# Optimization experiments

Measured on AMD Instinct MI355X. Metric: run time of the kernel, lower is better.

The kernel has to match this reference:

```python
import jax, jax.numpy as jnp
import numpy as np

B, T, I, H, L, O = 2048, 512, 1, 64, 2, 1


def _lstm_layer(x, Wih, Whh, b):
    """Single LSTM layer, batch_first x: [B, T, in] -> [B, T, H].
    PyTorch gate order: i, f, g, o. b = b_ih + b_hh (folded)."""
    Bn = x.shape[0]
    Hn = Whh.shape[1]
    # Precompute input contribution for all timesteps (hoisted out of scan)
    xg = jnp.einsum('bti,gi->btg', x, Wih) + b  # [B, T, 4H]

    def step(carry, xg_t):
        h, c = carry
        g = xg_t + h @ Whh.T  # [B, 4H]
        i, f, gg, o = jnp.split(g, 4, axis=-1)
        i = jax.nn.sigmoid(i)
        f = jax.nn.sigmoid(f)
        gg = jnp.tanh(gg)
        o = jax.nn.sigmoid(o)
        c = f * c + i * gg
        h = o * jnp.tanh(c)
        return (h, c), h

    h0 = jnp.zeros((Bn, Hn), x.dtype)
    c0 = jnp.zeros((Bn, Hn), x.dtype)
    (_, _), hs = jax.lax.scan(step, (h0, c0), jnp.swapaxes(xg, 0, 1))  # hs: [T, B, H]
    return jnp.swapaxes(hs, 0, 1)


def setup_inputs() -> dict:
    key = jax.random.key(0)
    ks = jax.random.split(key, 11)
    s = 1.0 / np.sqrt(H)  # torch default uniform bound
    u = lambda k, shp: jax.random.uniform(k, shp, jnp.float32, -s, s)
    return {
        'x': jax.random.normal(ks[0], (B, T, I), jnp.float32),
        'Wih0': u(ks[1], (4 * H, I)),
        'Whh0': u(ks[2], (4 * H, H)),
        'bih0': u(ks[3], (4 * H,)),
        'bhh0': u(ks[4], (4 * H,)),
        'Wih1': u(ks[5], (4 * H, H)),
        'Whh1': u(ks[6], (4 * H, H)),
        'bih1': u(ks[7], (4 * H,)),
        'bhh1': u(ks[8], (4 * H,)),
        'fcW': u(ks[9], (O, H)),
        'fcb': u(ks[10], (O,)),
    }


def reference(x, Wih0, Whh0, bih0, bhh0, Wih1, Whh1, bih1, bhh1, fcW, fcb):
    h1 = _lstm_layer(x, Wih0, Whh0, bih0 + bhh0)   # [B, T, H]
    h2 = _lstm_layer(h1, Wih1, Whh1, bih1 + bhh1)  # [B, T, H]
    return h2[:, -1, :] @ fcW.T + fcb               # [B, O]
```

## Files before the change

kernel.cpp:

```cpp
#include <hip/hip_runtime.h>


#define TT 512
#define HH 64
#define BT 8

typedef __attribute__((ext_vector_type(4))) int i32x4;

#define MFMAI8 __builtin_amdgcn_mfma_i32_16x16x64_i8

#define WSCALE 260096.0f
#define HSCALE 32512.0f
#define LOG2E  1.44269504f
constexpr float C_SIG = (float)(256.0 / (260096.0 * 32512.0) * 1.4426950408889634);
constexpr float C_TGH = (float)(2.0 * 256.0 / (260096.0 * 32512.0) * 1.4426950408889634);

__device__ __forceinline__ float exp2_hw(float x) {
    float r; asm("v_exp_f32 %0, %1" : "=v"(r) : "v"(x)); return r;
}
__device__ __forceinline__ float exp2n_hw(float x) {
    float r; asm("v_exp_f32 %0, -%1" : "=v"(r) : "v"(x)); return r;
}
__device__ __forceinline__ float gate4f(float p0, float p1, float p2, float p3, float& c) {
    float ia = exp2n_hw(p0);
    float fb = exp2n_hw(p1);
    float gb = exp2_hw(p2);
    float ob = exp2n_hw(p3);
    float A = 1.f + ia, B = 1.f + gb, F = 1.f + fb;
    float t1  = A * B;
    float den = t1 * F;
    float num = fmaf(c, t1, (B - 2.f) * F);
    c = num * __builtin_amdgcn_rcpf(den);
    float e2 = exp2_hw(fminf(c * (2.f * LOG2E), 126.f));
    float C  = 1.f + e2;
    float r2 = __builtin_amdgcn_rcpf((1.f + ob) * C);
    return (C - 2.f) * r2;
}
__device__ __forceinline__ int dpp_ror8_i(int v) {
    return __builtin_amdgcn_update_dpp(v, v, 0x128, 0xF, 0xF, true);
}
__device__ __forceinline__ void cvtW16(const float* __restrict__ p, i32x4& hi, i32x4& lo) {
    #pragma unroll
    for (int r = 0; r < 4; ++r) {
        int hw = 0, lw = 0;
        #pragma unroll
        for (int b = 0; b < 4; ++b) {
            int wq = (int)rintf(p[4 * b + r] * WSCALE);
            int h8 = (wq + 128) >> 8;
            int l8 = wq - (h8 << 8);
            hw |= (h8 & 0xFF) << (8 * b);
            lw |= (l8 & 0xFF) << (8 * b);
        }
        hi[r] = hw; lo[r] = lw;
    }
}

__global__ __launch_bounds__(512) void lstm_mfma(
    const float* __restrict__ x,
    const float* __restrict__ Wih0, const float* __restrict__ Whh0,
    const float* __restrict__ bih0, const float* __restrict__ bhh0,
    const float* __restrict__ Wih1, const float* __restrict__ Whh1,
    const float* __restrict__ bih1, const float* __restrict__ bhh1,
    const float* __restrict__ fcW, const float* __restrict__ fcb,
    float* __restrict__ out)
{
    __shared__ float xs[BT][TT + 1];
    __shared__ __align__(16) signed char aH[2][2][2][64][16];
    __shared__ float hF[BT][HH + 1];
    __shared__ float fcw_s[HH];

    const int t    = threadIdx.x;
    const int lane = t & 63;
    const int v    = t >> 6;
    const int b0   = blockIdx.x * BT;
    const int m    = lane & 15;
    const int q    = lane >> 4;
    const int ts   = m >> 3;
    const int bpk  = m & 7;
    const int j    = 4 * (2 * v + ts) + q;

    for (int i = t; i < BT * TT; i += 512)
        xs[i >> 9][i & (TT - 1)] = x[(size_t)(b0 + (i >> 9)) * TT + (i & (TT - 1))];
    {
        int* z = (int*)aH;
        for (int i = t; i < 2048; i += 512)
            z[i] = ((i >> 8) & 1) ? 0x80808080 : 0;
    }
    if (t < HH) fcw_s[t] = fcW[t];

    i32x4 A0h[2], A0l[2], I1h[2], I1l[2], H1h[2], H1l[2];
    #pragma unroll
    for (int i = 0; i < 2; ++i) {
        const int rho = (m & 3) * 64 + 4 * (2 * v + i) + (m >> 2);
        cvtW16(Whh0 + rho * HH + q * 16, A0h[i], A0l[i]);
        cvtW16(Wih1 + rho * HH + q * 16, I1h[i], I1l[i]);
        cvtW16(Whh1 + rho * HH + q * 16, H1h[i], H1l[i]);
    }

    i32x4 corrA[2], corrBI[2], corrBH[2];
    {
        i32x4 ones; ones[0] = 0x01010101; ones[1] = 0x01010101;
        ones[2] = 0x01010101; ones[3] = 0x01010101;
        i32x4 zz = {0, 0, 0, 0};
        #pragma unroll
        for (int i = 0; i < 2; ++i) {
            i32x4 Sa = MFMAI8(A0h[i], ones, zz, 0, 0, 0);
            i32x4 Si = MFMAI8(I1h[i], ones, zz, 0, 0, 0);
            i32x4 Sh = MFMAI8(H1h[i], ones, zz, 0, 0, 0);
            #pragma unroll
            for (int r = 0; r < 4; ++r) {
                corrA[i][r]  = Sa[r] << 7;
                corrBI[i][r] = Si[r] << 7;
                corrBH[i][r] = Sh[r] << 7;
            }
        }
    }

    float wxb[4], bia1[4], bia2[4];
    #pragma unroll
    for (int g = 0; g < 4; ++g) {
        const int r = g * 64 + j;
        const float sc = (g == 2) ? 2.f * LOG2E : LOG2E;
        wxb[g]  = Wih0[r] * sc;
        bia1[g] = (bih0[r] + bhh0[r]) * sc;
        bia2[g] = (bih1[r] + bhh1[r]) * sc;
    }
    const int wl = ((j >> 4) << 4) + bpk;
    const int wb = ((j & 3) << 2) | ((j >> 2) & 3);
    float c1 = 0.f, c2 = 0.f;

    __syncthreads();

    {
        i32x4 bh1 = *(const i32x4*)&aH[0][0][0][lane][0];
        i32x4 bl1 = *(const i32x4*)&aH[0][0][1][lane][0];
        i32x4 aHH[2], aMD[2];
        #pragma unroll
        for (int i = 0; i < 2; ++i) {
            i32x4 z4 = {0, 0, 0, 0};
            aHH[i] = MFMAI8(A0h[i], bh1, z4, 0, 0, 0);
            aMD[i] = MFMAI8(A0l[i], bh1, MFMAI8(A0h[i], bl1, corrA[i], 0, 0, 0), 0, 0, 0);
        }
        float xb = xs[bpk][0];
        float pre[4];
        #pragma unroll
        for (int r = 0; r < 4; ++r) {
            int Pa = (aHH[0][r] << 8) + aMD[0][r];
            int Pb = (aHH[1][r] << 8) + aMD[1][r];
            int P  = Pa + dpp_ror8_i(Pb);
            const float Cr = (r == 2) ? C_TGH : C_SIG;
            pre[r] = fmaf((float)P, Cr, fmaf(wxb[r], xb, bia1[r]));
        }
        float h1v = gate4f(pre[0], pre[1], pre[2], pre[3], c1);
        int u = __float_as_int(fmaf(h1v, HSCALE, 12582912.f));
        aH[0][1][0][wl][wb] = (signed char)(u >> 8);
        aH[0][1][1][wl][wb] = (signed char)(u ^ 0x80);
        __syncthreads();
    }

    #pragma unroll 2
    for (int k = 1; k < TT; ++k) {
        const int p = k & 1, pn = p ^ 1;
        i32x4 bh1 = *(const i32x4*)&aH[0][p][0][lane][0];
        i32x4 bl1 = *(const i32x4*)&aH[0][p][1][lane][0];
        i32x4 bh2 = *(const i32x4*)&aH[1][p][0][lane][0];
        i32x4 bl2 = *(const i32x4*)&aH[1][p][1][lane][0];
        float xb = xs[bpk][k];

        i32x4 aHH[2], aMD[2], bHH[2], bMD1[2], bMD2[2];
        #pragma unroll
        for (int i = 0; i < 2; ++i) {
            i32x4 z4 = {0, 0, 0, 0};
            aHH[i] = MFMAI8(A0h[i], bh1, z4, 0, 0, 0);
            aMD[i] = MFMAI8(A0l[i], bh1, MFMAI8(A0h[i], bl1, corrA[i], 0, 0, 0), 0, 0, 0);
        }
        #pragma unroll
        for (int i = 0; i < 2; ++i) {
            i32x4 z4 = {0, 0, 0, 0};
            bHH[i]  = MFMAI8(H1h[i], bh2, MFMAI8(I1h[i], bh1, z4, 0, 0, 0), 0, 0, 0);
            bMD1[i] = MFMAI8(I1l[i], bh1, MFMAI8(I1h[i], bl1, corrBI[i], 0, 0, 0), 0, 0, 0);
            bMD2[i] = MFMAI8(H1l[i], bh2, MFMAI8(H1h[i], bl2, corrBH[i], 0, 0, 0), 0, 0, 0);
        }
        __builtin_amdgcn_sched_barrier(0);

        {
            float pre[4];
            #pragma unroll
            for (int r = 0; r < 4; ++r) {
                int Pa = (aHH[0][r] << 8) + aMD[0][r];
                int Pb = (aHH[1][r] << 8) + aMD[1][r];
                int P  = Pa + dpp_ror8_i(Pb);
                const float Cr = (r == 2) ? C_TGH : C_SIG;
                pre[r] = fmaf((float)P, Cr, fmaf(wxb[r], xb, bia1[r]));
            }
            float h1v = gate4f(pre[0], pre[1], pre[2], pre[3], c1);
            int u = __float_as_int(fmaf(h1v, HSCALE, 12582912.f));
            aH[0][pn][0][wl][wb] = (signed char)(u >> 8);
            aH[0][pn][1][wl][wb] = (signed char)(u ^ 0x80);
        }
        {
            float pre[4];
            #pragma unroll
            for (int r = 0; r < 4; ++r) {
                int Pc = (bHH[0][r] << 8) + bMD1[0][r] + bMD2[0][r];
                int Pd = (bHH[1][r] << 8) + bMD1[1][r] + bMD2[1][r];
                int P  = Pc + dpp_ror8_i(Pd);
                const float Cr = (r == 2) ? C_TGH : C_SIG;
                pre[r] = fmaf((float)P, Cr, bia2[r]);
            }
            float h2v = gate4f(pre[0], pre[1], pre[2], pre[3], c2);
            int u = __float_as_int(fmaf(h2v, HSCALE, 12582912.f));
            aH[1][pn][0][wl][wb] = (signed char)(u >> 8);
            aH[1][pn][1][wl][wb] = (signed char)(u ^ 0x80);
        }
        __syncthreads();
    }

    {
        i32x4 bh1 = *(const i32x4*)&aH[0][0][0][lane][0];
        i32x4 bl1 = *(const i32x4*)&aH[0][0][1][lane][0];
        i32x4 bh2 = *(const i32x4*)&aH[1][0][0][lane][0];
        i32x4 bl2 = *(const i32x4*)&aH[1][0][1][lane][0];
        i32x4 bHH[2], bMD1[2], bMD2[2];
        #pragma unroll
        for (int i = 0; i < 2; ++i) {
            i32x4 z4 = {0, 0, 0, 0};
            bHH[i]  = MFMAI8(H1h[i], bh2, MFMAI8(I1h[i], bh1, z4, 0, 0, 0), 0, 0, 0);
            bMD1[i] = MFMAI8(I1l[i], bh1, MFMAI8(I1h[i], bl1, corrBI[i], 0, 0, 0), 0, 0, 0);
            bMD2[i] = MFMAI8(H1l[i], bh2, MFMAI8(H1h[i], bl2, corrBH[i], 0, 0, 0), 0, 0, 0);
        }
        float pre[4];
        #pragma unroll
        for (int r = 0; r < 4; ++r) {
            int Pc = (bHH[0][r] << 8) + bMD1[0][r] + bMD2[0][r];
            int Pd = (bHH[1][r] << 8) + bMD1[1][r] + bMD2[1][r];
            int P  = Pc + dpp_ror8_i(Pd);
            const float Cr = (r == 2) ? C_TGH : C_SIG;
            pre[r] = fmaf((float)P, Cr, bia2[r]);
        }
        float h2v = gate4f(pre[0], pre[1], pre[2], pre[3], c2);
        hF[bpk][j] = h2v;
    }
    __syncthreads();

    if (t < BT) {
        float s = fcb[0];
        #pragma unroll 8
        for (int jj = 0; jj < HH; ++jj)
            s = fmaf(hF[t][jj], fcw_s[jj], s);
        out[b0 + t] = s;
    }
}

extern "C" void kernel_launch(void* const* d_in, const int* in_sizes, int n_in,
                              void* d_out, int out_size, void* d_ws, size_t ws_size,
                              hipStream_t stream) {
    const float* x    = (const float*)d_in[0];
    const float* Wih0 = (const float*)d_in[1];
    const float* Whh0 = (const float*)d_in[2];
    const float* bih0 = (const float*)d_in[3];
    const float* bhh0 = (const float*)d_in[4];
    const float* Wih1 = (const float*)d_in[5];
    const float* Whh1 = (const float*)d_in[6];
    const float* bih1 = (const float*)d_in[7];
    const float* bhh1 = (const float*)d_in[8];
    const float* fcW  = (const float*)d_in[9];
    const float* fcb  = (const float*)d_in[10];
    float* out = (float*)d_out;

    lstm_mfma<<<dim3(2048 / BT), dim3(512), 0, stream>>>(
        x, Wih0, Whh0, bih0, bhh0, Wih1, Whh1, bih1, bhh1, fcW, fcb, out);
}
```

Baseline: 458.1 us.

## Fold zero-point correction into biases, chain MFMAs, request two blocks per CU

```diff
diff --git a/kernel.cpp b/kernel.cpp
--- a/kernel.cpp
+++ b/kernel.cpp
@@ -55,7 +55,7 @@
     }
 }
 
-__global__ __launch_bounds__(512) void lstm_mfma(
+__global__ __launch_bounds__(512, 2) void lstm_mfma(
     const float* __restrict__ x,
     const float* __restrict__ Wih0, const float* __restrict__ Whh0,
     const float* __restrict__ bih0, const float* __restrict__ bhh0,
@@ -97,25 +97,6 @@
         cvtW16(Whh1 + rho * HH + q * 16, H1h[i], H1l[i]);
     }
 
-    i32x4 corrA[2], corrBI[2], corrBH[2];
-    {
-        i32x4 ones; ones[0] = 0x01010101; ones[1] = 0x01010101;
-        ones[2] = 0x01010101; ones[3] = 0x01010101;
-        i32x4 zz = {0, 0, 0, 0};
-        #pragma unroll
-        for (int i = 0; i < 2; ++i) {
-            i32x4 Sa = MFMAI8(A0h[i], ones, zz, 0, 0, 0);
-            i32x4 Si = MFMAI8(I1h[i], ones, zz, 0, 0, 0);
-            i32x4 Sh = MFMAI8(H1h[i], ones, zz, 0, 0, 0);
-            #pragma unroll
-            for (int r = 0; r < 4; ++r) {
-                corrA[i][r]  = Sa[r] << 7;
-                corrBI[i][r] = Si[r] << 7;
-                corrBH[i][r] = Sh[r] << 7;
-            }
-        }
-    }
-
     float wxb[4], bia1[4], bia2[4];
     #pragma unroll
     for (int g = 0; g < 4; ++g) {
@@ -125,9 +106,29 @@
         bia1[g] = (bih0[r] + bhh0[r]) * sc;
         bia2[g] = (bih1[r] + bhh1[r]) * sc;
     }
+
+    {
+        i32x4 ones; ones[0] = 0x01010101; ones[1] = 0x01010101;
+        ones[2] = 0x01010101; ones[3] = 0x01010101;
+        i32x4 zz = {0, 0, 0, 0};
+        i32x4 Sa0 = MFMAI8(A0h[0], ones, zz, 0, 0, 0);
+        i32x4 Sa1 = MFMAI8(A0h[1], ones, zz, 0, 0, 0);
+        i32x4 Sb0 = MFMAI8(H1h[0], ones, MFMAI8(I1h[0], ones, zz, 0, 0, 0), 0, 0, 0);
+        i32x4 Sb1 = MFMAI8(H1h[1], ones, MFMAI8(I1h[1], ones, zz, 0, 0, 0), 0, 0, 0);
+        #pragma unroll
+        for (int g = 0; g < 4; ++g) {
+            const float Cg = (g == 2) ? C_TGH : C_SIG;
+            float cA = (float)((ts ? Sa1[g] : Sa0[g]) << 7);
+            float cB = (float)((ts ? Sb1[g] : Sb0[g]) << 7);
+            bia1[g] = fmaf(cA, Cg, bia1[g]);
+            bia2[g] = fmaf(cB, Cg, bia2[g]);
+        }
+    }
+
     const int wl = ((j >> 4) << 4) + bpk;
     const int wb = ((j & 3) << 2) | ((j >> 2) & 3);
     float c1 = 0.f, c2 = 0.f;
+    const i32x4 z4 = {0, 0, 0, 0};
 
     __syncthreads();
 
@@ -137,9 +138,8 @@
         i32x4 aHH[2], aMD[2];
         #pragma unroll
         for (int i = 0; i < 2; ++i) {
-            i32x4 z4 = {0, 0, 0, 0};
             aHH[i] = MFMAI8(A0h[i], bh1, z4, 0, 0, 0);
-            aMD[i] = MFMAI8(A0l[i], bh1, MFMAI8(A0h[i], bl1, corrA[i], 0, 0, 0), 0, 0, 0);
+            aMD[i] = MFMAI8(A0l[i], bh1, MFMAI8(A0h[i], bl1, z4, 0, 0, 0), 0, 0, 0);
         }
         float xb = xs[bpk][0];
         float pre[4];
@@ -167,19 +167,19 @@
         i32x4 bl2 = *(const i32x4*)&aH[1][p][1][lane][0];
         float xb = xs[bpk][k];
 
-        i32x4 aHH[2], aMD[2], bHH[2], bMD1[2], bMD2[2];
-        #pragma unroll
-        for (int i = 0; i < 2; ++i) {
-            i32x4 z4 = {0, 0, 0, 0};
+        i32x4 aHH[2], aMD[2], bHH[2], bMD[2];
+        #pragma unroll
+        for (int i = 0; i < 2; ++i) {
             aHH[i] = MFMAI8(A0h[i], bh1, z4, 0, 0, 0);
-            aMD[i] = MFMAI8(A0l[i], bh1, MFMAI8(A0h[i], bl1, corrA[i], 0, 0, 0), 0, 0, 0);
-        }
-        #pragma unroll
-        for (int i = 0; i < 2; ++i) {
-            i32x4 z4 = {0, 0, 0, 0};
-            bHH[i]  = MFMAI8(H1h[i], bh2, MFMAI8(I1h[i], bh1, z4, 0, 0, 0), 0, 0, 0);
-            bMD1[i] = MFMAI8(I1l[i], bh1, MFMAI8(I1h[i], bl1, corrBI[i], 0, 0, 0), 0, 0, 0);
-            bMD2[i] = MFMAI8(H1l[i], bh2, MFMAI8(H1h[i], bl2, corrBH[i], 0, 0, 0), 0, 0, 0);
+            aMD[i] = MFMAI8(A0l[i], bh1, MFMAI8(A0h[i], bl1, z4, 0, 0, 0), 0, 0, 0);
+        }
+        #pragma unroll
+        for (int i = 0; i < 2; ++i) {
+            bHH[i] = MFMAI8(H1h[i], bh2, MFMAI8(I1h[i], bh1, z4, 0, 0, 0), 0, 0, 0);
+            bMD[i] = MFMAI8(H1l[i], bh2,
+                     MFMAI8(H1h[i], bl2,
+                     MFMAI8(I1l[i], bh1,
+                     MFMAI8(I1h[i], bl1, z4, 0, 0, 0), 0, 0, 0), 0, 0, 0), 0, 0, 0);
         }
         __builtin_amdgcn_sched_barrier(0);
 
@@ -198,12 +198,14 @@
             aH[0][pn][0][wl][wb] = (signed char)(u >> 8);
             aH[0][pn][1][wl][wb] = (signed char)(u ^ 0x80);
         }
+        __builtin_amdgcn_sched_barrier(0);
+
         {
             float pre[4];
             #pragma unroll
             for (int r = 0; r < 4; ++r) {
-                int Pc = (bHH[0][r] << 8) + bMD1[0][r] + bMD2[0][r];
-                int Pd = (bHH[1][r] << 8) + bMD1[1][r] + bMD2[1][r];
+                int Pc = (bHH[0][r] << 8) + bMD[0][r];
+                int Pd = (bHH[1][r] << 8) + bMD[1][r];
                 int P  = Pc + dpp_ror8_i(Pd);
                 const float Cr = (r == 2) ? C_TGH : C_SIG;
                 pre[r] = fmaf((float)P, Cr, bia2[r]);
@@ -221,19 +223,20 @@
         i32x4 bl1 = *(const i32x4*)&aH[0][0][1][lane][0];
         i32x4 bh2 = *(const i32x4*)&aH[1][0][0][lane][0];
         i32x4 bl2 = *(const i32x4*)&aH[1][0][1][lane][0];
-        i32x4 bHH[2], bMD1[2], bMD2[2];
-        #pragma unroll
-        for (int i = 0; i < 2; ++i) {
-            i32x4 z4 = {0, 0, 0, 0};
-            bHH[i]  = MFMAI8(H1h[i], bh2, MFMAI8(I1h[i], bh1, z4, 0, 0, 0), 0, 0, 0);
-            bMD1[i] = MFMAI8(I1l[i], bh1, MFMAI8(I1h[i], bl1, corrBI[i], 0, 0, 0), 0, 0, 0);
-            bMD2[i] = MFMAI8(H1l[i], bh2, MFMAI8(H1h[i], bl2, corrBH[i], 0, 0, 0), 0, 0, 0);
+        i32x4 bHH[2], bMD[2];
+        #pragma unroll
+        for (int i = 0; i < 2; ++i) {
+            bHH[i] = MFMAI8(H1h[i], bh2, MFMAI8(I1h[i], bh1, z4, 0, 0, 0), 0, 0, 0);
+            bMD[i] = MFMAI8(H1l[i], bh2,
+                     MFMAI8(H1h[i], bl2,
+                     MFMAI8(I1l[i], bh1,
+                     MFMAI8(I1h[i], bl1, z4, 0, 0, 0), 0, 0, 0), 0, 0, 0), 0, 0, 0);
         }
         float pre[4];
         #pragma unroll
         for (int r = 0; r < 4; ++r) {
-            int Pc = (bHH[0][r] << 8) + bMD1[0][r] + bMD2[0][r];
-            int Pd = (bHH[1][r] << 8) + bMD1[1][r] + bMD2[1][r];
+            int Pc = (bHH[0][r] << 8) + bMD[0][r];
+            int Pd = (bHH[1][r] << 8) + bMD[1][r];
             int P  = Pc + dpp_ror8_i(Pd);
             const float Cr = (r == 2) ? C_TGH : C_SIG;
             pre[r] = fmaf((float)P, Cr, bia2[r]);
```

New measurement: 428.3 us. -6.5%, faster.
